# Optimization experiments

Measured on AMD Instinct MI355X. Metric: run time of the kernel, lower is better.

Reference implementation:

```python
import jax, jax.numpy as jnp
import numpy as np

C = 1536          # interim_dim
D2 = 2 * C        # 3072, fc_nlb dim
LN_EPS = 1e-5


def setup_inputs() -> dict:
    key = jax.random.key(0)
    ks = jax.random.split(key, 24)
    B, L = 32, 1024
    s = 0.02
    inp = {
        "x": jax.random.normal(ks[0], (B, C), dtype=jnp.float32),
        "lfb_feats": jax.random.normal(ks[1], (B, L, C), dtype=jnp.float32),
        # 1x1 Conv1d weights act as (C_out, C_in) matmuls
        "theta_w": jax.random.normal(ks[2], (C, C), dtype=jnp.float32) * s,
        "theta_b": jnp.zeros((C,), dtype=jnp.float32),
        "phi_w": jax.random.normal(ks[3], (C, C), dtype=jnp.float32) * s,
        "phi_b": jnp.zeros((C,), dtype=jnp.float32),
        "gi_w": jax.random.normal(ks[4], (C, C), dtype=jnp.float32) * s,
        "gi_b": jnp.zeros((C,), dtype=jnp.float32),
        "ln_g": jnp.ones((C,), dtype=jnp.float32),
        "ln_b": jnp.zeros((C,), dtype=jnp.float32),
        "fc_w": jax.random.normal(ks[5], (C, C), dtype=jnp.float32) * s,
        "fc_b": jnp.zeros((C,), dtype=jnp.float32),
        "fc_nlb_w": jax.random.normal(ks[6], (D2, D2), dtype=jnp.float32) * s,
        "fc_nlb_b": jnp.zeros((D2,), dtype=jnp.float32),
        "fc1_w": jax.random.normal(ks[7], (1, 1024), dtype=jnp.float32) * s,
        "fc1_b": jnp.zeros((1,), dtype=jnp.float32),
        "fc2_w": jax.random.normal(ks[8], (1, 1024), dtype=jnp.float32) * s,
        "fc2_b": jnp.zeros((1,), dtype=jnp.float32),
        "fc3_w": jax.random.normal(ks[9], (1, 1024), dtype=jnp.float32) * s,
        "fc3_b": jnp.zeros((1,), dtype=jnp.float32),
        "fct_w": jax.random.normal(ks[10], (1, D2), dtype=jnp.float32) * s,
        "fct_b": jnp.zeros((1,), dtype=jnp.float32),
    }
    return inp


def _layernorm(x, g, b):
    mu = jnp.mean(x, axis=-1, keepdims=True)
    var = jnp.mean(jnp.square(x - mu), axis=-1, keepdims=True)
    return (x - mu) * jax.lax.rsqrt(var + LN_EPS) * g + b


def reference(x, lfb_feats, theta_w, theta_b, phi_w, phi_b, gi_w, gi_b,
              ln_g, ln_b, fc_w, fc_b, fc_nlb_w, fc_nlb_b,
              fc1_w, fc1_b, fc2_w, fc2_b, fc3_w, fc3_b, fct_w, fct_b):
    # --- _NLBlock on feats = x.unsqueeze(1): query sequence length is 1 ---
    # note: scale = 1/sqrt(1/C) = sqrt(C) (as in the original code)
    scale = jnp.sqrt(jnp.asarray(C, dtype=x.dtype))
    theta = x @ theta_w.T + theta_b                       # (B, C)
    phi = lfb_feats @ phi_w.T + phi_b                     # (B, L, C)
    gi = lfb_feats @ gi_w.T + gi_b                        # (B, L, C)
    scores = jnp.einsum('bc,blc->bl', theta, phi) * scale  # (B, L)
    attn = jax.nn.softmax(scores, axis=-1)
    o = jnp.einsum('bl,blc->bc', attn, gi)                # (B, C)
    o = jax.nn.relu(_layernorm(o, ln_g, ln_b))
    o = o @ fc_w.T + fc_b                                 # dropout -> identity (eval)
    longterm = o + x                                      # residual, (B, C)

    # --- head ---
    feats = jnp.concatenate([x, longterm], axis=1)        # (B, 2C)
    feats = jax.nn.relu(feats @ fc_nlb_w.T + fc_nlb_b)    # dropout -> identity
    f1 = feats[:, :1024]
    f2 = feats[:, 1024:2048]
    f3 = feats[:, 2048:3072]
    p1 = f1 @ fc1_w.T + fc1_b
    p2 = f2 @ fc2_w.T + fc2_b
    p3 = f3 @ fc3_w.T + fc3_b
    pt = feats @ fct_w.T + fct_b
    return jnp.concatenate([p1, p2, p3, pt], axis=1)      # (B, 4)
```

## Files before the change

kernel.cpp:

```cpp
#include <hip/hip_runtime.h>
#include <math.h>

#define B 32
#define C 1536
#define D2 3072
#define L 1024
#define KC 64
#define CH 16
#define LPW 16

__device__ inline float dot4(float4 a, float4 b) {
    return a.x * b.x + a.y * b.y + a.z * b.z + a.w * b.w;
}
__device__ inline float4 ld4(const float* p) { return *(const float4*)p; }
__device__ inline void   st4(float* p, float4 v) { *(float4*)p = v; }

__device__ inline int sw(int row, int q) {
    return row * KC + ((q ^ ((row >> 2) & 7)) << 2);
}

__global__ __launch_bounds__(256) void init_k(float* __restrict__ theta, const float* __restrict__ tb,
                                              float* __restrict__ u,
                                              float* __restrict__ obuf, const float* __restrict__ gib,
                                              float* __restrict__ o2, const float* __restrict__ fcb,
                                              float* __restrict__ h, const float* __restrict__ fcnb) {
    int i = blockIdx.x * 256 + threadIdx.x;
    if (i < 32 * C) {
        int j = i % C;
        theta[i] = tb[j];
        u[i]     = 0.f;
        obuf[i]  = gib[j];
        o2[i]    = fcb[j];
    }
    if (i < 32 * D2) h[i] = fcnb[i % D2];
}

__global__ __launch_bounds__(256) void gemm32(const float* __restrict__ A,
                                              const float* __restrict__ W,
                                              float* __restrict__ out,
                                              int N, int K, int kchunks) {
    __shared__ float xs[32 * KC];
    __shared__ float wsm[64 * KC];
    int tid = threadIdx.x;
    int j0 = blockIdx.x * 64;
    int kb = blockIdx.y;
    int tb = tid & 15;
    int tj = tid >> 4;

    float4 acc0 = make_float4(0.f, 0.f, 0.f, 0.f);
    float4 acc1 = make_float4(0.f, 0.f, 0.f, 0.f);

    for (int c = 0; c < kchunks; ++c) {
        int k0 = (kb * kchunks + c) * KC;
        __syncthreads();
        #pragma unroll
        for (int p = 0; p < 2; ++p) {
            int f = tid + 256 * p;
            int row = f >> 4, q = f & 15;
            st4(xs + sw(row, q), ld4(A + (size_t)row * K + k0 + 4 * q));
        }
        #pragma unroll
        for (int p = 0; p < 4; ++p) {
            int f = tid + 256 * p;
            int row = f >> 4, q = f & 15;
            st4(wsm + sw(row, q), ld4(W + (size_t)(j0 + row) * K + k0 + 4 * q));
        }
        __syncthreads();
        #pragma unroll
        for (int kq = 0; kq < 16; ++kq) {
            float4 x0 = ld4(xs + sw(2 * tb, kq));
            float4 x1 = ld4(xs + sw(2 * tb + 1, kq));
            float4 w0 = ld4(wsm + sw(4 * tj + 0, kq));
            float4 w1 = ld4(wsm + sw(4 * tj + 1, kq));
            float4 w2 = ld4(wsm + sw(4 * tj + 2, kq));
            float4 w3 = ld4(wsm + sw(4 * tj + 3, kq));
            acc0.x += dot4(x0, w0); acc0.y += dot4(x0, w1);
            acc0.z += dot4(x0, w2); acc0.w += dot4(x0, w3);
            acc1.x += dot4(x1, w0); acc1.y += dot4(x1, w1);
            acc1.z += dot4(x1, w2); acc1.w += dot4(x1, w3);
        }
    }
    float* p0 = out + (size_t)(2 * tb + 0) * N + j0 + 4 * tj;
    float* p1 = out + (size_t)(2 * tb + 1) * N + j0 + 4 * tj;
    atomicAdd(p0 + 0, acc0.x); atomicAdd(p0 + 1, acc0.y);
    atomicAdd(p0 + 2, acc0.z); atomicAdd(p0 + 3, acc0.w);
    atomicAdd(p1 + 0, acc1.x); atomicAdd(p1 + 1, acc1.y);
    atomicAdd(p1 + 2, acc1.z); atomicAdd(p1 + 3, acc1.w);
}

__global__ __launch_bounds__(256) void gemm32_nt(const float* __restrict__ A,
                                                 const float* __restrict__ W,
                                                 float* __restrict__ out,
                                                 int N, int K, int kchunks) {
    __shared__ float xs[32 * KC];
    __shared__ float wsm[64 * KC];
    int tid = threadIdx.x;
    int j0 = blockIdx.x * 64;
    int kb = blockIdx.y;
    int tb = tid & 15;
    int tj = tid >> 4;

    float4 acc0 = make_float4(0.f, 0.f, 0.f, 0.f);
    float4 acc1 = make_float4(0.f, 0.f, 0.f, 0.f);

    for (int c = 0; c < kchunks; ++c) {
        int k0 = (kb * kchunks + c) * KC;
        __syncthreads();
        #pragma unroll
        for (int p = 0; p < 2; ++p) {
            int f = tid + 256 * p;
            int row = f >> 4, q = f & 15;
            st4(xs + sw(row, q), ld4(A + (size_t)row * K + k0 + 4 * q));
        }
        #pragma unroll
        for (int p = 0; p < 4; ++p) {
            int f = tid + 256 * p;
            int r = f >> 4;
            int cq = f & 15;
            float4 v = ld4(W + (size_t)(k0 + r) * N + j0 + 4 * cq);
            wsm[sw(4 * cq + 0, r >> 2) + (r & 3)] = v.x;
            wsm[sw(4 * cq + 1, r >> 2) + (r & 3)] = v.y;
            wsm[sw(4 * cq + 2, r >> 2) + (r & 3)] = v.z;
            wsm[sw(4 * cq + 3, r >> 2) + (r & 3)] = v.w;
        }
        __syncthreads();
        #pragma unroll
        for (int kq = 0; kq < 16; ++kq) {
            float4 x0 = ld4(xs + sw(2 * tb, kq));
            float4 x1 = ld4(xs + sw(2 * tb + 1, kq));
            float4 w0 = ld4(wsm + sw(4 * tj + 0, kq));
            float4 w1 = ld4(wsm + sw(4 * tj + 1, kq));
            float4 w2 = ld4(wsm + sw(4 * tj + 2, kq));
            float4 w3 = ld4(wsm + sw(4 * tj + 3, kq));
            acc0.x += dot4(x0, w0); acc0.y += dot4(x0, w1);
            acc0.z += dot4(x0, w2); acc0.w += dot4(x0, w3);
            acc1.x += dot4(x1, w0); acc1.y += dot4(x1, w1);
            acc1.z += dot4(x1, w2); acc1.w += dot4(x1, w3);
        }
    }
    float* p0 = out + (size_t)(2 * tb + 0) * N + j0 + 4 * tj;
    float* p1 = out + (size_t)(2 * tb + 1) * N + j0 + 4 * tj;
    atomicAdd(p0 + 0, acc0.x); atomicAdd(p0 + 1, acc0.y);
    atomicAdd(p0 + 2, acc0.z); atomicAdd(p0 + 3, acc0.w);
    atomicAdd(p1 + 0, acc1.x); atomicAdd(p1 + 1, acc1.y);
    atomicAdd(p1 + 2, acc1.z); atomicAdd(p1 + 3, acc1.w);
}

__global__ __launch_bounds__(256) void gemm32_h(const float* __restrict__ x,
                                                const float* __restrict__ o2,
                                                const float* __restrict__ W,
                                                float* __restrict__ out,
                                                int N, int K, int kchunks) {
    __shared__ float xs[32 * KC];
    __shared__ float wsm[64 * KC];
    int tid = threadIdx.x;
    int j0 = blockIdx.x * 64;
    int kb = blockIdx.y;
    int tb = tid & 15;
    int tj = tid >> 4;

    float4 acc0 = make_float4(0.f, 0.f, 0.f, 0.f);
    float4 acc1 = make_float4(0.f, 0.f, 0.f, 0.f);

    for (int c = 0; c < kchunks; ++c) {
        int k0 = (kb * kchunks + c) * KC;
        __syncthreads();
        #pragma unroll
        for (int p = 0; p < 2; ++p) {
            int f = tid + 256 * p;
            int row = f >> 4, q = f & 15;
            int kk = k0 + 4 * q;
            float4 v;
            if (kk < C) {
                v = ld4(x + (size_t)row * C + kk);
            } else {
                float4 a = ld4(x + (size_t)row * C + kk - C);
                float4 b = ld4(o2 + (size_t)row * C + kk - C);
                v = make_float4(a.x + b.x, a.y + b.y, a.z + b.z, a.w + b.w);
            }
            st4(xs + sw(row, q), v);
        }
        #pragma unroll
        for (int p = 0; p < 4; ++p) {
            int f = tid + 256 * p;
            int row = f >> 4, q = f & 15;
            st4(wsm + sw(row, q), ld4(W + (size_t)(j0 + row) * K + k0 + 4 * q));
        }
        __syncthreads();
        #pragma unroll
        for (int kq = 0; kq < 16; ++kq) {
            float4 x0 = ld4(xs + sw(2 * tb, kq));
            float4 x1 = ld4(xs + sw(2 * tb + 1, kq));
            float4 w0 = ld4(wsm + sw(4 * tj + 0, kq));
            float4 w1 = ld4(wsm + sw(4 * tj + 1, kq));
            float4 w2 = ld4(wsm + sw(4 * tj + 2, kq));
            float4 w3 = ld4(wsm + sw(4 * tj + 3, kq));
            acc0.x += dot4(x0, w0); acc0.y += dot4(x0, w1);
            acc0.z += dot4(x0, w2); acc0.w += dot4(x0, w3);
            acc1.x += dot4(x1, w0); acc1.y += dot4(x1, w1);
            acc1.z += dot4(x1, w2); acc1.w += dot4(x1, w3);
        }
    }
    float* p0 = out + (size_t)(2 * tb + 0) * N + j0 + 4 * tj;
    float* p1 = out + (size_t)(2 * tb + 1) * N + j0 + 4 * tj;
    atomicAdd(p0 + 0, acc0.x); atomicAdd(p0 + 1, acc0.y);
    atomicAdd(p0 + 2, acc0.z); atomicAdd(p0 + 3, acc0.w);
    atomicAdd(p1 + 0, acc1.x); atomicAdd(p1 + 1, acc1.y);
    atomicAdd(p1 + 2, acc1.z); atomicAdd(p1 + 3, acc1.w);
}

__global__ __launch_bounds__(256) void ln_relu(const float* __restrict__ obuf,
                                               const float* __restrict__ g,
                                               const float* __restrict__ bt,
                                               float* __restrict__ out) {
    int b = blockIdx.x, tid = threadIdx.x;
    __shared__ float r1[4], r2[4];
    float lv[6];
    float s1 = 0.f, s2 = 0.f;
    #pragma unroll
    for (int t = 0; t < 6; ++t) {
        int c = tid + 256 * t;
        float acc = obuf[(size_t)b * C + c];
        lv[t] = acc; s1 += acc; s2 += acc * acc;
    }
    #pragma unroll
    for (int off = 32; off > 0; off >>= 1) {
        s1 += __shfl_xor(s1, off, 64);
        s2 += __shfl_xor(s2, off, 64);
    }
    int wave = tid >> 6, lane = tid & 63;
    if (lane == 0) { r1[wave] = s1; r2[wave] = s2; }
    __syncthreads();
    s1 = r1[0] + r1[1] + r1[2] + r1[3];
    s2 = r2[0] + r2[1] + r2[2] + r2[3];
    float mu = s1 / (float)C;
    float var = s2 / (float)C - mu * mu;
    float rstd = 1.0f / sqrtf(var + 1e-5f);
    #pragma unroll
    for (int t = 0; t < 6; ++t) {
        int c = tid + 256 * t;
        float y = (lv[t] - mu) * rstd * g[c] + bt[c];
        out[(size_t)b * C + c] = fmaxf(y, 0.f);
    }
}

__global__ __launch_bounds__(256) void flash_k(const float* __restrict__ u,
                                               const float* __restrict__ lfb,
                                               float* __restrict__ pm,
                                               float* __restrict__ ps,
                                               float* __restrict__ pv) {
    int chunk = blockIdx.x;
    int b = blockIdx.y;
    int wave = threadIdx.x >> 6;
    int lane = threadIdx.x & 63;
    int widx = chunk * 4 + wave;

    const float scale = 39.19183588453085f;

    float uu[24];
    const float* ub = u + (size_t)b * C;
    #pragma unroll
    for (int t = 0; t < 6; ++t)
        *(float4*)(uu + 4 * t) = ld4(ub + 4 * lane + 256 * t);

    float m = -INFINITY, s = 0.f;
    float vv[24];
    #pragma unroll
    for (int t = 0; t < 24; ++t) vv[t] = 0.f;

    int l0 = chunk * (L / CH) + wave;
    for (int i = 0; i < LPW; ++i) {
        int l = l0 + i * 4;
        const float* row = lfb + ((size_t)b * L + l) * C;
        float xx[24];
        #pragma unroll
        for (int t = 0; t < 6; ++t)
            *(float4*)(xx + 4 * t) = ld4(row + 4 * lane + 256 * t);
        float d = 0.f;
        #pragma unroll
        for (int t = 0; t < 24; ++t) d += xx[t] * uu[t];
        #pragma unroll
        for (int off = 32; off > 0; off >>= 1) d += __shfl_xor(d, off, 64);
        float score = d * scale;
        float mn = fmaxf(m, score);
        float alpha = __expf(m - mn);
        float p = __expf(score - mn);
        s = s * alpha + p;
        #pragma unroll
        for (int t = 0; t < 24; ++t) vv[t] = vv[t] * alpha + p * xx[t];
        m = mn;
    }

    if (lane == 0) { pm[b * 64 + widx] = m; ps[b * 64 + widx] = s; }
    float* pvb = pv + ((size_t)b * 64 + widx) * C;
    #pragma unroll
    for (int t = 0; t < 6; ++t)
        st4(pvb + 4 * lane + 256 * t, *(float4*)(vv + 4 * t));
}

__global__ __launch_bounds__(256) void combine_k(const float* __restrict__ pm,
                                                 const float* __restrict__ ps,
                                                 const float* __restrict__ pv,
                                                 float* __restrict__ v) {
    int cc = blockIdx.x;
    int b = blockIdx.y;
    int tid = threadIdx.x;
    __shared__ float coef[64];
    if (tid < 64) {
        float mj = pm[b * 64 + tid];
        float M = mj;
        #pragma unroll
        for (int off = 32; off > 0; off >>= 1) M = fmaxf(M, __shfl_xor(M, off, 64));
        float ej = expf(mj - M);
        float S = ps[b * 64 + tid] * ej;
        #pragma unroll
        for (int off = 32; off > 0; off >>= 1) S += __shfl_xor(S, off, 64);
        coef[tid] = ej / S;
    }
    __syncthreads();
    int c = cc * 256 + tid;
    float acc = 0.f;
    #pragma unroll 8
    for (int j = 0; j < 64; ++j)
        acc += coef[j] * pv[((size_t)b * 64 + j) * C + c];
    v[(size_t)b * C + c] = acc;
}

__global__ __launch_bounds__(256) void final_k(const float* __restrict__ h,
                                               const float* __restrict__ w1, const float* __restrict__ b1,
                                               const float* __restrict__ w2, const float* __restrict__ b2,
                                               const float* __restrict__ w3, const float* __restrict__ b3,
                                               const float* __restrict__ wt, const float* __restrict__ bt,
                                               float* __restrict__ out) {
    int b = blockIdx.x;
    int tid = threadIdx.x;
    float ph0 = 0.f, ph1 = 0.f, ph2 = 0.f, ptv = 0.f;
    #pragma unroll
    for (int t = 0; t < 12; ++t) {
        int j = tid + 256 * t;
        float s = fmaxf(h[(size_t)b * D2 + j], 0.f);
        ptv += s * wt[j];
        int jj = tid + 256 * (t & 3);
        if (t < 4)       ph0 += s * w1[jj];
        else if (t < 8)  ph1 += s * w2[jj];
        else             ph2 += s * w3[jj];
    }
    #pragma unroll
    for (int off = 32; off > 0; off >>= 1) {
        ph0 += __shfl_xor(ph0, off, 64);
        ph1 += __shfl_xor(ph1, off, 64);
        ph2 += __shfl_xor(ph2, off, 64);
        ptv += __shfl_xor(ptv, off, 64);
    }
    __shared__ float red[4][4];
    int wave = tid >> 6, lane = tid & 63;
    if (lane == 0) {
        red[wave][0] = ph0; red[wave][1] = ph1; red[wave][2] = ph2; red[wave][3] = ptv;
    }
    __syncthreads();
    if (tid < 4) {
        float v = red[0][tid] + red[1][tid] + red[2][tid] + red[3][tid];
        float bias = (tid == 0) ? b1[0] : (tid == 1) ? b2[0] : (tid == 2) ? b3[0] : bt[0];
        out[b * 4 + tid] = v + bias;
    }
}

extern "C" void kernel_launch(void* const* d_in, const int* in_sizes, int n_in,
                              void* d_out, int out_size, void* d_ws, size_t ws_size,
                              hipStream_t stream) {
    (void)in_sizes; (void)n_in; (void)out_size; (void)ws_size;
    const float* x       = (const float*)d_in[0];
    const float* lfb     = (const float*)d_in[1];
    const float* theta_w = (const float*)d_in[2];
    const float* theta_b = (const float*)d_in[3];
    const float* phi_w   = (const float*)d_in[4];
    const float* gi_w    = (const float*)d_in[6];
    const float* gi_b    = (const float*)d_in[7];
    const float* ln_g    = (const float*)d_in[8];
    const float* ln_b    = (const float*)d_in[9];
    const float* fc_w    = (const float*)d_in[10];
    const float* fc_b    = (const float*)d_in[11];
    const float* fcn_w   = (const float*)d_in[12];
    const float* fcn_b   = (const float*)d_in[13];
    const float* w1 = (const float*)d_in[14]; const float* b1 = (const float*)d_in[15];
    const float* w2 = (const float*)d_in[16]; const float* b2 = (const float*)d_in[17];
    const float* w3 = (const float*)d_in[18]; const float* b3 = (const float*)d_in[19];
    const float* wt = (const float*)d_in[20]; const float* bt = (const float*)d_in[21];
    float* out = (float*)d_out;
    float* w = (float*)d_ws;

    float* pv    = w;
    float* pm    = w + 3145728;
    float* ps    = w + 3147776;
    float* theta = w + 3149824;
    float* u     = w + 3198976;
    float* vbuf  = w + 3248128;
    float* obuf  = w + 3297280;
    float* oln   = w + 3346432;
    float* o2    = w + 3395584;
    float* h     = w + 3444736;

    init_k<<<384, 256, 0, stream>>>(theta, theta_b, u, obuf, gi_b, o2, fc_b, h, fcn_b);

    gemm32<<<dim3(24, 12), 256, 0, stream>>>(x, theta_w, theta, C, C, 2);

    gemm32_nt<<<dim3(24, 12), 256, 0, stream>>>(theta, phi_w, u, C, C, 2);

    flash_k<<<dim3(CH, B), 256, 0, stream>>>(u, lfb, pm, ps, pv);
    combine_k<<<dim3(6, B), 256, 0, stream>>>(pm, ps, pv, vbuf);

    gemm32<<<dim3(24, 12), 256, 0, stream>>>(vbuf, gi_w, obuf, C, C, 2);
    ln_relu<<<B, 256, 0, stream>>>(obuf, ln_g, ln_b, oln);

    gemm32<<<dim3(24, 12), 256, 0, stream>>>(oln, fc_w, o2, C, C, 2);

    gemm32_h<<<dim3(48, 12), 256, 0, stream>>>(x, o2, fcn_w, h, D2, D2, 4);

    final_k<<<B, 256, 0, stream>>>(h, w1, b1, w2, b2, w3, b3, wt, bt, out);
}
```

Before: 477.7 us.

## Fuse all stages into one persistent megakernel with grid barriers

Replaces the sequence of separate kernel launches with a single persistent kernel of 512 blocks that runs every stage and separates them with atomic-counter grid barriers. Split-K GEMM results are no longer accumulated with global atomics into pre-initialised buffers. Each K-slice writes its own partial tile, and a reduction stage sums the slices and adds the bias, which also removes the init kernel. This is meant to cut launch and inter-kernel gaps and atomic traffic, at the cost of extra barrier stages, partial-buffer memory traffic, and reliance on all 512 blocks being co-resident (two per CU).

```diff
diff --git a/kernel.cpp b/kernel.cpp
--- a/kernel.cpp
+++ b/kernel.cpp
@@ -1,11 +1,12 @@
 #include <hip/hip_runtime.h>
 #include <math.h>
 
-#define B 32
 #define C 1536
 #define D2 3072
 #define L 1024
 #define KC 64
+#define NB 512
+#define NT 256
 #define CH 16
 #define LPW 16
 
@@ -19,50 +20,49 @@
     return row * KC + ((q ^ ((row >> 2) & 7)) << 2);
 }
 
-__global__ __launch_bounds__(256) void init_k(float* __restrict__ theta, const float* __restrict__ tb,
-                                              float* __restrict__ u,
-                                              float* __restrict__ obuf, const float* __restrict__ gib,
-                                              float* __restrict__ o2, const float* __restrict__ fcb,
-                                              float* __restrict__ h, const float* __restrict__ fcnb) {
-    int i = blockIdx.x * 256 + threadIdx.x;
-    if (i < 32 * C) {
-        int j = i % C;
-        theta[i] = tb[j];
-        u[i]     = 0.f;
-        obuf[i]  = gib[j];
-        o2[i]    = fcb[j];
-    }
-    if (i < 32 * D2) h[i] = fcnb[i % D2];
-}
-
-__global__ __launch_bounds__(256) void gemm32(const float* __restrict__ A,
-                                              const float* __restrict__ W,
-                                              float* __restrict__ out,
-                                              int N, int K, int kchunks) {
-    __shared__ float xs[32 * KC];
-    __shared__ float wsm[64 * KC];
+struct Params {
+    const float *x, *lfb, *theta_w, *theta_b, *phi_w, *gi_w, *gi_b;
+    const float *ln_g, *ln_b, *fc_w, *fc_b, *fcn_w, *fcn_b;
+    const float *w1, *b1, *w2, *b2, *w3, *b3, *wt, *bt;
+    float *out;
+    float *part, *partH, *pv, *pm, *ps, *theta, *u, *vbuf, *oln, *lt;
+    unsigned *bar;
+};
+
+__device__ inline void gridbar(unsigned* bar, int idx) {
+    __syncthreads();
+    if (threadIdx.x == 0) {
+        __threadfence();
+        __hip_atomic_fetch_add(&bar[idx], 1u, __ATOMIC_ACQ_REL, __HIP_MEMORY_SCOPE_AGENT);
+        int spins = 0;
+        while (__hip_atomic_load(&bar[idx], __ATOMIC_ACQUIRE, __HIP_MEMORY_SCOPE_AGENT) < NB) {
+            __builtin_amdgcn_s_sleep(4);
+            if (++spins > (1 << 20)) break;
+        }
+        __threadfence();
+    }
+    __syncthreads();
+}
+
+__device__ void gemm_nn(const float* __restrict__ A, const float* __restrict__ W,
+                        float* __restrict__ part, int N, int K, int kchunks,
+                        int jt, int kb, float* xs, float* wsm) {
     int tid = threadIdx.x;
-    int j0 = blockIdx.x * 64;
-    int kb = blockIdx.y;
-    int tb = tid & 15;
-    int tj = tid >> 4;
-
+    int j0 = jt * 64;
+    int tb = tid & 15, tj = tid >> 4;
     float4 acc0 = make_float4(0.f, 0.f, 0.f, 0.f);
     float4 acc1 = make_float4(0.f, 0.f, 0.f, 0.f);
-
     for (int c = 0; c < kchunks; ++c) {
         int k0 = (kb * kchunks + c) * KC;
         __syncthreads();
         #pragma unroll
         for (int p = 0; p < 2; ++p) {
-            int f = tid + 256 * p;
-            int row = f >> 4, q = f & 15;
+            int f = tid + 256 * p, row = f >> 4, q = f & 15;
             st4(xs + sw(row, q), ld4(A + (size_t)row * K + k0 + 4 * q));
         }
         #pragma unroll
         for (int p = 0; p < 4; ++p) {
-            int f = tid + 256 * p;
-            int row = f >> 4, q = f & 15;
+            int f = tid + 256 * p, row = f >> 4, q = f & 15;
             st4(wsm + sw(row, q), ld4(W + (size_t)(j0 + row) * K + k0 + 4 * q));
         }
         __syncthreads();
@@ -80,36 +80,24 @@
             acc1.z += dot4(x1, w2); acc1.w += dot4(x1, w3);
         }
     }
-    float* p0 = out + (size_t)(2 * tb + 0) * N + j0 + 4 * tj;
-    float* p1 = out + (size_t)(2 * tb + 1) * N + j0 + 4 * tj;
-    atomicAdd(p0 + 0, acc0.x); atomicAdd(p0 + 1, acc0.y);
-    atomicAdd(p0 + 2, acc0.z); atomicAdd(p0 + 3, acc0.w);
-    atomicAdd(p1 + 0, acc1.x); atomicAdd(p1 + 1, acc1.y);
-    atomicAdd(p1 + 2, acc1.z); atomicAdd(p1 + 3, acc1.w);
-}
-
-__global__ __launch_bounds__(256) void gemm32_nt(const float* __restrict__ A,
-                                                 const float* __restrict__ W,
-                                                 float* __restrict__ out,
-                                                 int N, int K, int kchunks) {
-    __shared__ float xs[32 * KC];
-    __shared__ float wsm[64 * KC];
+    st4(part + ((size_t)kb * 32 + 2 * tb + 0) * N + j0 + 4 * tj, acc0);
+    st4(part + ((size_t)kb * 32 + 2 * tb + 1) * N + j0 + 4 * tj, acc1);
+}
+
+__device__ void gemm_nt(const float* __restrict__ A, const float* __restrict__ W,
+                        float* __restrict__ part, int N, int K, int kchunks,
+                        int jt, int kb, float* xs, float* wsm) {
     int tid = threadIdx.x;
-    int j0 = blockIdx.x * 64;
-    int kb = blockIdx.y;
-    int tb = tid & 15;
-    int tj = tid >> 4;
-
+    int j0 = jt * 64;
+    int tb = tid & 15, tj = tid >> 4;
     float4 acc0 = make_float4(0.f, 0.f, 0.f, 0.f);
     float4 acc1 = make_float4(0.f, 0.f, 0.f, 0.f);
-
     for (int c = 0; c < kchunks; ++c) {
         int k0 = (kb * kchunks + c) * KC;
         __syncthreads();
         #pragma unroll
         for (int p = 0; p < 2; ++p) {
-            int f = tid + 256 * p;
-            int row = f >> 4, q = f & 15;
+            int f = tid + 256 * p, row = f >> 4, q = f & 15;
             st4(xs + sw(row, q), ld4(A + (size_t)row * K + k0 + 4 * q));
         }
         #pragma unroll
@@ -138,53 +126,33 @@
             acc1.z += dot4(x1, w2); acc1.w += dot4(x1, w3);
         }
     }
-    float* p0 = out + (size_t)(2 * tb + 0) * N + j0 + 4 * tj;
-    float* p1 = out + (size_t)(2 * tb + 1) * N + j0 + 4 * tj;
-    atomicAdd(p0 + 0, acc0.x); atomicAdd(p0 + 1, acc0.y);
-    atomicAdd(p0 + 2, acc0.z); atomicAdd(p0 + 3, acc0.w);
-    atomicAdd(p1 + 0, acc1.x); atomicAdd(p1 + 1, acc1.y);
-    atomicAdd(p1 + 2, acc1.z); atomicAdd(p1 + 3, acc1.w);
-}
-
-__global__ __launch_bounds__(256) void gemm32_h(const float* __restrict__ x,
-                                                const float* __restrict__ o2,
-                                                const float* __restrict__ W,
-                                                float* __restrict__ out,
-                                                int N, int K, int kchunks) {
-    __shared__ float xs[32 * KC];
-    __shared__ float wsm[64 * KC];
+    st4(part + ((size_t)kb * 32 + 2 * tb + 0) * N + j0 + 4 * tj, acc0);
+    st4(part + ((size_t)kb * 32 + 2 * tb + 1) * N + j0 + 4 * tj, acc1);
+}
+
+__device__ void gemm_feats(const float* __restrict__ x, const float* __restrict__ lt,
+                           const float* __restrict__ W, float* __restrict__ part,
+                           int jt, int kb, float* xs, float* wsm) {
     int tid = threadIdx.x;
-    int j0 = blockIdx.x * 64;
-    int kb = blockIdx.y;
-    int tb = tid & 15;
-    int tj = tid >> 4;
-
+    int j0 = jt * 64;
+    int tb = tid & 15, tj = tid >> 4;
     float4 acc0 = make_float4(0.f, 0.f, 0.f, 0.f);
     float4 acc1 = make_float4(0.f, 0.f, 0.f, 0.f);
-
-    for (int c = 0; c < kchunks; ++c) {
-        int k0 = (kb * kchunks + c) * KC;
+    for (int c = 0; c < 4; ++c) {
+        int k0 = (kb * 4 + c) * KC;
         __syncthreads();
         #pragma unroll
         for (int p = 0; p < 2; ++p) {
-            int f = tid + 256 * p;
-            int row = f >> 4, q = f & 15;
+            int f = tid + 256 * p, row = f >> 4, q = f & 15;
             int kk = k0 + 4 * q;
-            float4 v;
-            if (kk < C) {
-                v = ld4(x + (size_t)row * C + kk);
-            } else {
-                float4 a = ld4(x + (size_t)row * C + kk - C);
-                float4 b = ld4(o2 + (size_t)row * C + kk - C);
-                v = make_float4(a.x + b.x, a.y + b.y, a.z + b.z, a.w + b.w);
-            }
+            float4 v = (kk < C) ? ld4(x + (size_t)row * C + kk)
+                                : ld4(lt + (size_t)row * C + kk - C);
             st4(xs + sw(row, q), v);
         }
         #pragma unroll
         for (int p = 0; p < 4; ++p) {
-            int f = tid + 256 * p;
-            int row = f >> 4, q = f & 15;
-            st4(wsm + sw(row, q), ld4(W + (size_t)(j0 + row) * K + k0 + 4 * q));
+            int f = tid + 256 * p, row = f >> 4, q = f & 15;
+            st4(wsm + sw(row, q), ld4(W + (size_t)(j0 + row) * D2 + k0 + 4 * q));
         }
         __syncthreads();
         #pragma unroll
@@ -201,26 +169,108 @@
             acc1.z += dot4(x1, w2); acc1.w += dot4(x1, w3);
         }
     }
-    float* p0 = out + (size_t)(2 * tb + 0) * N + j0 + 4 * tj;
-    float* p1 = out + (size_t)(2 * tb + 1) * N + j0 + 4 * tj;
-    atomicAdd(p0 + 0, acc0.x); atomicAdd(p0 + 1, acc0.y);
-    atomicAdd(p0 + 2, acc0.z); atomicAdd(p0 + 3, acc0.w);
-    atomicAdd(p1 + 0, acc1.x); atomicAdd(p1 + 1, acc1.y);
-    atomicAdd(p1 + 2, acc1.z); atomicAdd(p1 + 3, acc1.w);
-}
-
-__global__ __launch_bounds__(256) void ln_relu(const float* __restrict__ obuf,
-                                               const float* __restrict__ g,
-                                               const float* __restrict__ bt,
-                                               float* __restrict__ out) {
+    st4(part + ((size_t)kb * 32 + 2 * tb + 0) * D2 + j0 + 4 * tj, acc0);
+    st4(part + ((size_t)kb * 32 + 2 * tb + 1) * D2 + j0 + 4 * tj, acc1);
+}
+
+__device__ inline void reduce12(const float* __restrict__ part, const float* __restrict__ bias,
+                                const float* __restrict__ addx, float* __restrict__ outp) {
+    int i = blockIdx.x * NT + threadIdx.x;
+    if (i < 32 * C) {
+        int b = i / C, j = i - b * C;
+        float s = 0.f;
+        #pragma unroll
+        for (int kk = 0; kk < 12; ++kk) s += part[((size_t)kk * 32 + b) * C + j];
+        if (bias) s += bias[j];
+        if (addx) s += addx[i];
+        outp[i] = s;
+    }
+}
+
+__device__ void flash_stage(const Params& p) {
+    int gid = blockIdx.x;
+    int b = gid & 31, chunk = gid >> 5;
+    int wave = threadIdx.x >> 6, lane = threadIdx.x & 63;
+    int widx = chunk * 4 + wave;
+
+    const float scale = 39.19183588453085f;
+
+    float uu[24];
+    const float* ub = p.u + (size_t)b * C;
+    #pragma unroll
+    for (int t = 0; t < 6; ++t)
+        *(float4*)(uu + 4 * t) = ld4(ub + 4 * lane + 256 * t);
+
+    float m = -INFINITY, s = 0.f;
+    float vv[24];
+    #pragma unroll
+    for (int t = 0; t < 24; ++t) vv[t] = 0.f;
+
+    int l0 = chunk * (L / CH) + wave;
+    for (int i = 0; i < LPW; ++i) {
+        int l = l0 + i * 4;
+        const float* row = p.lfb + ((size_t)b * L + l) * C;
+        float xx[24];
+        #pragma unroll
+        for (int t = 0; t < 6; ++t)
+            *(float4*)(xx + 4 * t) = ld4(row + 4 * lane + 256 * t);
+        float d = 0.f;
+        #pragma unroll
+        for (int t = 0; t < 24; ++t) d += xx[t] * uu[t];
+        #pragma unroll
+        for (int off = 32; off > 0; off >>= 1) d += __shfl_xor(d, off, 64);
+        float score = d * scale;
+        float mn = fmaxf(m, score);
+        float alpha = __expf(m - mn);
+        float pr = __expf(score - mn);
+        s = s * alpha + pr;
+        #pragma unroll
+        for (int t = 0; t < 24; ++t) vv[t] = vv[t] * alpha + pr * xx[t];
+        m = mn;
+    }
+
+    if (lane == 0) { p.pm[b * 64 + widx] = m; p.ps[b * 64 + widx] = s; }
+    float* pvb = p.pv + ((size_t)b * 64 + widx) * C;
+    #pragma unroll
+    for (int t = 0; t < 6; ++t)
+        st4(pvb + 4 * lane + 256 * t, *(float4*)(vv + 4 * t));
+}
+
+__device__ void combine_stage(const Params& p, float* coef) {
+    int gid = blockIdx.x;
+    int b = gid & 31, cc = gid >> 5;
+    int tid = threadIdx.x;
+    if (tid < 64) {
+        float mj = p.pm[b * 64 + tid];
+        float M = mj;
+        #pragma unroll
+        for (int off = 32; off > 0; off >>= 1) M = fmaxf(M, __shfl_xor(M, off, 64));
+        float ej = expf(mj - M);
+        float S = p.ps[b * 64 + tid] * ej;
+        #pragma unroll
+        for (int off = 32; off > 0; off >>= 1) S += __shfl_xor(S, off, 64);
+        coef[tid] = ej / S;
+    }
+    __syncthreads();
+    int c = cc * 256 + tid;
+    float acc = 0.f;
+    #pragma unroll 8
+    for (int j = 0; j < 64; ++j)
+        acc += coef[j] * p.pv[((size_t)b * 64 + j) * C + c];
+    p.vbuf[(size_t)b * C + c] = acc;
+}
+
+__device__ void ln_stage(const Params& p, float* r1, float* r2) {
     int b = blockIdx.x, tid = threadIdx.x;
-    __shared__ float r1[4], r2[4];
     float lv[6];
     float s1 = 0.f, s2 = 0.f;
     #pragma unroll
     for (int t = 0; t < 6; ++t) {
         int c = tid + 256 * t;
-        float acc = obuf[(size_t)b * C + c];
+        float acc = 0.f;
+        #pragma unroll
+        for (int kk = 0; kk < 12; ++kk) acc += p.part[((size_t)kk * 32 + b) * C + c];
+        acc += p.gi_b[c];
         lv[t] = acc; s1 += acc; s2 += acc * acc;
     }
     #pragma unroll
@@ -239,111 +289,28 @@
     #pragma unroll
     for (int t = 0; t < 6; ++t) {
         int c = tid + 256 * t;
-        float y = (lv[t] - mu) * rstd * g[c] + bt[c];
-        out[(size_t)b * C + c] = fmaxf(y, 0.f);
-    }
-}
-
-__global__ __launch_bounds__(256) void flash_k(const float* __restrict__ u,
-                                               const float* __restrict__ lfb,
-                                               float* __restrict__ pm,
-                                               float* __restrict__ ps,
-                                               float* __restrict__ pv) {
-    int chunk = blockIdx.x;
-    int b = blockIdx.y;
-    int wave = threadIdx.x >> 6;
-    int lane = threadIdx.x & 63;
-    int widx = chunk * 4 + wave;
-
-    const float scale = 39.19183588453085f;
-
-    float uu[24];
-    const float* ub = u + (size_t)b * C;
-    #pragma unroll
-    for (int t = 0; t < 6; ++t)
-        *(float4*)(uu + 4 * t) = ld4(ub + 4 * lane + 256 * t);
-
-    float m = -INFINITY, s = 0.f;
-    float vv[24];
-    #pragma unroll
-    for (int t = 0; t < 24; ++t) vv[t] = 0.f;
-
-    int l0 = chunk * (L / CH) + wave;
-    for (int i = 0; i < LPW; ++i) {
-        int l = l0 + i * 4;
-        const float* row = lfb + ((size_t)b * L + l) * C;
-        float xx[24];
-        #pragma unroll
-        for (int t = 0; t < 6; ++t)
-            *(float4*)(xx + 4 * t) = ld4(row + 4 * lane + 256 * t);
-        float d = 0.f;
-        #pragma unroll
-        for (int t = 0; t < 24; ++t) d += xx[t] * uu[t];
-        #pragma unroll
-        for (int off = 32; off > 0; off >>= 1) d += __shfl_xor(d, off, 64);
-        float score = d * scale;
-        float mn = fmaxf(m, score);
-        float alpha = __expf(m - mn);
-        float p = __expf(score - mn);
-        s = s * alpha + p;
-        #pragma unroll
-        for (int t = 0; t < 24; ++t) vv[t] = vv[t] * alpha + p * xx[t];
-        m = mn;
-    }
-
-    if (lane == 0) { pm[b * 64 + widx] = m; ps[b * 64 + widx] = s; }
-    float* pvb = pv + ((size_t)b * 64 + widx) * C;
-    #pragma unroll
-    for (int t = 0; t < 6; ++t)
-        st4(pvb + 4 * lane + 256 * t, *(float4*)(vv + 4 * t));
-}
-
-__global__ __launch_bounds__(256) void combine_k(const float* __restrict__ pm,
-                                                 const float* __restrict__ ps,
-                                                 const float* __restrict__ pv,
-                                                 float* __restrict__ v) {
-    int cc = blockIdx.x;
-    int b = blockIdx.y;
-    int tid = threadIdx.x;
-    __shared__ float coef[64];
-    if (tid < 64) {
-        float mj = pm[b * 64 + tid];
-        float M = mj;
-        #pragma unroll
-        for (int off = 32; off > 0; off >>= 1) M = fmaxf(M, __shfl_xor(M, off, 64));
-        float ej = expf(mj - M);
-        float S = ps[b * 64 + tid] * ej;
-        #pragma unroll
-        for (int off = 32; off > 0; off >>= 1) S += __shfl_xor(S, off, 64);
-        coef[tid] = ej / S;
-    }
-    __syncthreads();
-    int c = cc * 256 + tid;
-    float acc = 0.f;
-    #pragma unroll 8
-    for (int j = 0; j < 64; ++j)
-        acc += coef[j] * pv[((size_t)b * 64 + j) * C + c];
-    v[(size_t)b * C + c] = acc;
-}
-
-__global__ __launch_bounds__(256) void final_k(const float* __restrict__ h,
-                                               const float* __restrict__ w1, const float* __restrict__ b1,
-                                               const float* __restrict__ w2, const float* __restrict__ b2,
-                                               const float* __restrict__ w3, const float* __restrict__ b3,
-                                               const float* __restrict__ wt, const float* __restrict__ bt,
-                                               float* __restrict__ out) {
-    int b = blockIdx.x;
-    int tid = threadIdx.x;
+        float y = (lv[t] - mu) * rstd * p.ln_g[c] + p.ln_b[c];
+        p.oln[(size_t)b * C + c] = fmaxf(y, 0.f);
+    }
+}
+
+__device__ void final_stage(const Params& p, float* red) {
+    int b = blockIdx.x, tid = threadIdx.x;
     float ph0 = 0.f, ph1 = 0.f, ph2 = 0.f, ptv = 0.f;
     #pragma unroll
     for (int t = 0; t < 12; ++t) {
         int j = tid + 256 * t;
-        float s = fmaxf(h[(size_t)b * D2 + j], 0.f);
-        ptv += s * wt[j];
+        float s = 0.f;
+        #pragma unroll
+        for (int ss = 0; ss < 12; ++ss)
+            s += p.partH[((size_t)ss * 32 + b) * D2 + j];
+        s += p.fcn_b[j];
+        s = fmaxf(s, 0.f);
+        ptv += s * p.wt[j];
         int jj = tid + 256 * (t & 3);
-        if (t < 4)       ph0 += s * w1[jj];
-        else if (t < 8)  ph1 += s * w2[jj];
-        else             ph2 += s * w3[jj];
+        if (t < 4)       ph0 += s * p.w1[jj];
+        else if (t < 8)  ph1 += s * p.w2[jj];
+        else             ph2 += s * p.w3[jj];
     }
     #pragma unroll
     for (int off = 32; off > 0; off >>= 1) {
@@ -352,69 +319,90 @@
         ph2 += __shfl_xor(ph2, off, 64);
         ptv += __shfl_xor(ptv, off, 64);
     }
-    __shared__ float red[4][4];
     int wave = tid >> 6, lane = tid & 63;
     if (lane == 0) {
-        red[wave][0] = ph0; red[wave][1] = ph1; red[wave][2] = ph2; red[wave][3] = ptv;
+        red[wave * 4 + 0] = ph0; red[wave * 4 + 1] = ph1;
+        red[wave * 4 + 2] = ph2; red[wave * 4 + 3] = ptv;
     }
     __syncthreads();
     if (tid < 4) {
-        float v = red[0][tid] + red[1][tid] + red[2][tid] + red[3][tid];
-        float bias = (tid == 0) ? b1[0] : (tid == 1) ? b2[0] : (tid == 2) ? b3[0] : bt[0];
-        out[b * 4 + tid] = v + bias;
-    }
+        float v = red[0 * 4 + tid] + red[1 * 4 + tid] + red[2 * 4 + tid] + red[3 * 4 + tid];
+        float bias = (tid == 0) ? p.b1[0] : (tid == 1) ? p.b2[0] : (tid == 2) ? p.b3[0] : p.bt[0];
+        p.out[b * 4 + tid] = v + bias;
+    }
+}
+
+__global__ __launch_bounds__(NT, 2) void mega(Params p) {
+    __shared__ float smem[6144];
+    float* xs = smem;
+    float* wsm = smem + 2048;
+    int gid = blockIdx.x;
+
+    if (gid < 288) gemm_nn(p.x, p.theta_w, p.part, C, C, 2, gid / 12, gid % 12, xs, wsm);
+    gridbar(p.bar, 0);
+    reduce12(p.part, p.theta_b, nullptr, p.theta);
+    gridbar(p.bar, 1);
+    if (gid < 288) gemm_nt(p.theta, p.phi_w, p.part, C, C, 2, gid / 12, gid % 12, xs, wsm);
+    gridbar(p.bar, 2);
+    reduce12(p.part, nullptr, nullptr, p.u);
+    gridbar(p.bar, 3);
+    flash_stage(p);
+    gridbar(p.bar, 4);
+    if (gid < 192) combine_stage(p, smem);
+    gridbar(p.bar, 5);
+    if (gid < 288) gemm_nn(p.vbuf, p.gi_w, p.part, C, C, 2, gid / 12, gid % 12, xs, wsm);
+    gridbar(p.bar, 6);
+    if (gid < 32) ln_stage(p, smem, smem + 8);
+    gridbar(p.bar, 7);
+    if (gid < 288) gemm_nn(p.oln, p.fc_w, p.part, C, C, 2, gid / 12, gid % 12, xs, wsm);
+    gridbar(p.bar, 8);
+    reduce12(p.part, p.fc_b, p.x, p.lt);
+    gridbar(p.bar, 9);
+    for (int t = gid; t < 576; t += NB)
+        gemm_feats(p.x, p.lt, p.fcn_w, p.partH, t / 12, t % 12, xs, wsm);
+    gridbar(p.bar, 10);
+    if (gid < 32) final_stage(p, smem);
 }
 
 extern "C" void kernel_launch(void* const* d_in, const int* in_sizes, int n_in,
                               void* d_out, int out_size, void* d_ws, size_t ws_size,
                               hipStream_t stream) {
     (void)in_sizes; (void)n_in; (void)out_size; (void)ws_size;
-    const float* x       = (const float*)d_in[0];
-    const float* lfb     = (const float*)d_in[1];
-    const float* theta_w = (const float*)d_in[2];
-    const float* theta_b = (const float*)d_in[3];
-    const float* phi_w   = (const float*)d_in[4];
-    const float* gi_w    = (const float*)d_in[6];
-    const float* gi_b    = (const float*)d_in[7];
-    const float* ln_g    = (const float*)d_in[8];
-    const float* ln_b    = (const float*)d_in[9];
-    const float* fc_w    = (const float*)d_in[10];
-    const float* fc_b    = (const float*)d_in[11];
-    const float* fcn_w   = (const float*)d_in[12];
-    const float* fcn_b   = (const float*)d_in[13];
-    const float* w1 = (const float*)d_in[14]; const float* b1 = (const float*)d_in[15];
-    const float* w2 = (const float*)d_in[16]; const float* b2 = (const float*)d_in[17];
-    const float* w3 = (const float*)d_in[18]; const float* b3 = (const float*)d_in[19];
-    const float* wt = (const float*)d_in[20]; const float* bt = (const float*)d_in[21];
-    float* out = (float*)d_out;
     float* w = (float*)d_ws;
 
-    float* pv    = w;
-    float* pm    = w + 3145728;
-    float* ps    = w + 3147776;
-    float* theta = w + 3149824;
-    float* u     = w + 3198976;
-    float* vbuf  = w + 3248128;
-    float* obuf  = w + 3297280;
-    float* oln   = w + 3346432;
-    float* o2    = w + 3395584;
-    float* h     = w + 3444736;
-
-    init_k<<<384, 256, 0, stream>>>(theta, theta_b, u, obuf, gi_b, o2, fc_b, h, fcn_b);
-
-    gemm32<<<dim3(24, 12), 256, 0, stream>>>(x, theta_w, theta, C, C, 2);
-
-    gemm32_nt<<<dim3(24, 12), 256, 0, stream>>>(theta, phi_w, u, C, C, 2);
-
-    flash_k<<<dim3(CH, B), 256, 0, stream>>>(u, lfb, pm, ps, pv);
-    combine_k<<<dim3(6, B), 256, 0, stream>>>(pm, ps, pv, vbuf);
-
-    gemm32<<<dim3(24, 12), 256, 0, stream>>>(vbuf, gi_w, obuf, C, C, 2);
-    ln_relu<<<B, 256, 0, stream>>>(obuf, ln_g, ln_b, oln);
-
-    gemm32<<<dim3(24, 12), 256, 0, stream>>>(oln, fc_w, o2, C, C, 2);
-
-    gemm32_h<<<dim3(48, 12), 256, 0, stream>>>(x, o2, fcn_w, h, D2, D2, 4);
-
-    final_k<<<B, 256, 0, stream>>>(h, w1, b1, w2, b2, w3, b3, wt, bt, out);
-}
+    Params p;
+    p.x       = (const float*)d_in[0];
+    p.lfb     = (const float*)d_in[1];
+    p.theta_w = (const float*)d_in[2];
+    p.theta_b = (const float*)d_in[3];
+    p.phi_w   = (const float*)d_in[4];
+    p.gi_w    = (const float*)d_in[6];
+    p.gi_b    = (const float*)d_in[7];
+    p.ln_g    = (const float*)d_in[8];
+    p.ln_b    = (const float*)d_in[9];
+    p.fc_w    = (const float*)d_in[10];
+    p.fc_b    = (const float*)d_in[11];
+    p.fcn_w   = (const float*)d_in[12];
+    p.fcn_b   = (const float*)d_in[13];
+    p.w1 = (const float*)d_in[14]; p.b1 = (const float*)d_in[15];
+    p.w2 = (const float*)d_in[16]; p.b2 = (const float*)d_in[17];
+    p.w3 = (const float*)d_in[18]; p.b3 = (const float*)d_in[19];
+    p.wt = (const float*)d_in[20]; p.bt = (const float*)d_in[21];
+    p.out = (float*)d_out;
+
+    p.part  = w;
+    p.partH = w + 589824;
+    p.pv    = w + 1769472;
+    p.pm    = w + 4915200;
+    p.ps    = w + 4917248;
+    p.theta = w + 4919296;
+    p.u     = w + 4968448;
+    p.vbuf  = w + 5017600;
+    p.oln   = w + 5066752;
+    p.lt    = w + 5115904;
+    p.bar   = (unsigned*)(w + 5165056);
+
+    hipMemsetAsync((void*)p.bar, 0, 64, stream);
+
+    mega<<<dim3(NB), dim3(NT), 0, stream>>>(p);
+}
```

After: 1.458 ms. +205.2%, slower.

## Replace atomic split-K accumulation with partial buffers reduced in consumer kernels

Applied to the files above, without the earlier changes.

Each split-K GEMM now writes its per-slice partial sums to a dedicated buffer instead of atomically adding into a pre-initialized output. The 12-way reduction plus bias is folded into the loading stage of the next kernel (gemm_u, flash_k, reduce_ln_relu, gemm_h, final_k), and the init kernel is removed. This removes atomic traffic and one launch. In exchange, every consumer re-reads 12 partials, several times over across blocks, which adds memory traffic.

```diff
diff --git a/kernel.cpp b/kernel.cpp
--- a/kernel.cpp
+++ b/kernel.cpp
@@ -19,25 +19,19 @@
     return row * KC + ((q ^ ((row >> 2) & 7)) << 2);
 }
 
-__global__ __launch_bounds__(256) void init_k(float* __restrict__ theta, const float* __restrict__ tb,
-                                              float* __restrict__ u,
-                                              float* __restrict__ obuf, const float* __restrict__ gib,
-                                              float* __restrict__ o2, const float* __restrict__ fcb,
-                                              float* __restrict__ h, const float* __restrict__ fcnb) {
-    int i = blockIdx.x * 256 + threadIdx.x;
-    if (i < 32 * C) {
-        int j = i % C;
-        theta[i] = tb[j];
-        u[i]     = 0.f;
-        obuf[i]  = gib[j];
-        o2[i]    = fcb[j];
-    }
-    if (i < 32 * D2) h[i] = fcnb[i % D2];
+__device__ inline float4 sum12(const float* __restrict__ part, int row, int col, int N) {
+    float4 s = ld4(part + (size_t)row * N + col);
+    #pragma unroll
+    for (int kk = 1; kk < 12; ++kk) {
+        float4 t = ld4(part + ((size_t)kk * 32 + row) * N + col);
+        s.x += t.x; s.y += t.y; s.z += t.z; s.w += t.w;
+    }
+    return s;
 }
 
 __global__ __launch_bounds__(256) void gemm32(const float* __restrict__ A,
                                               const float* __restrict__ W,
-                                              float* __restrict__ out,
+                                              float* __restrict__ part,
                                               int N, int K, int kchunks) {
     __shared__ float xs[32 * KC];
     __shared__ float wsm[64 * KC];
@@ -80,44 +74,43 @@
             acc1.z += dot4(x1, w2); acc1.w += dot4(x1, w3);
         }
     }
-    float* p0 = out + (size_t)(2 * tb + 0) * N + j0 + 4 * tj;
-    float* p1 = out + (size_t)(2 * tb + 1) * N + j0 + 4 * tj;
-    atomicAdd(p0 + 0, acc0.x); atomicAdd(p0 + 1, acc0.y);
-    atomicAdd(p0 + 2, acc0.z); atomicAdd(p0 + 3, acc0.w);
-    atomicAdd(p1 + 0, acc1.x); atomicAdd(p1 + 1, acc1.y);
-    atomicAdd(p1 + 2, acc1.z); atomicAdd(p1 + 3, acc1.w);
-}
-
-__global__ __launch_bounds__(256) void gemm32_nt(const float* __restrict__ A,
-                                                 const float* __restrict__ W,
-                                                 float* __restrict__ out,
-                                                 int N, int K, int kchunks) {
+    st4(part + ((size_t)kb * 32 + 2 * tb + 0) * N + j0 + 4 * tj, acc0);
+    st4(part + ((size_t)kb * 32 + 2 * tb + 1) * N + j0 + 4 * tj, acc1);
+}
+
+__global__ __launch_bounds__(256) void gemm_u(const float* __restrict__ pT,
+                                              const float* __restrict__ tb_,
+                                              const float* __restrict__ W,
+                                              float* __restrict__ part) {
     __shared__ float xs[32 * KC];
     __shared__ float wsm[64 * KC];
     int tid = threadIdx.x;
     int j0 = blockIdx.x * 64;
     int kb = blockIdx.y;
-    int tb = tid & 15;
-    int tj = tid >> 4;
+    int tb = tid & 15, tj = tid >> 4;
 
     float4 acc0 = make_float4(0.f, 0.f, 0.f, 0.f);
     float4 acc1 = make_float4(0.f, 0.f, 0.f, 0.f);
 
-    for (int c = 0; c < kchunks; ++c) {
-        int k0 = (kb * kchunks + c) * KC;
+    for (int c = 0; c < 2; ++c) {
+        int k0 = (kb * 2 + c) * KC;
         __syncthreads();
         #pragma unroll
         for (int p = 0; p < 2; ++p) {
             int f = tid + 256 * p;
             int row = f >> 4, q = f & 15;
-            st4(xs + sw(row, q), ld4(A + (size_t)row * K + k0 + 4 * q));
+            int col = k0 + 4 * q;
+            float4 v = sum12(pT, row, col, C);
+            float4 b4 = ld4(tb_ + col);
+            v.x += b4.x; v.y += b4.y; v.z += b4.z; v.w += b4.w;
+            st4(xs + sw(row, q), v);
         }
         #pragma unroll
         for (int p = 0; p < 4; ++p) {
             int f = tid + 256 * p;
             int r = f >> 4;
             int cq = f & 15;
-            float4 v = ld4(W + (size_t)(k0 + r) * N + j0 + 4 * cq);
+            float4 v = ld4(W + (size_t)(k0 + r) * C + j0 + 4 * cq);
             wsm[sw(4 * cq + 0, r >> 2) + (r & 3)] = v.x;
             wsm[sw(4 * cq + 1, r >> 2) + (r & 3)] = v.y;
             wsm[sw(4 * cq + 2, r >> 2) + (r & 3)] = v.z;
@@ -138,32 +131,27 @@
             acc1.z += dot4(x1, w2); acc1.w += dot4(x1, w3);
         }
     }
-    float* p0 = out + (size_t)(2 * tb + 0) * N + j0 + 4 * tj;
-    float* p1 = out + (size_t)(2 * tb + 1) * N + j0 + 4 * tj;
-    atomicAdd(p0 + 0, acc0.x); atomicAdd(p0 + 1, acc0.y);
-    atomicAdd(p0 + 2, acc0.z); atomicAdd(p0 + 3, acc0.w);
-    atomicAdd(p1 + 0, acc1.x); atomicAdd(p1 + 1, acc1.y);
-    atomicAdd(p1 + 2, acc1.z); atomicAdd(p1 + 3, acc1.w);
-}
-
-__global__ __launch_bounds__(256) void gemm32_h(const float* __restrict__ x,
-                                                const float* __restrict__ o2,
-                                                const float* __restrict__ W,
-                                                float* __restrict__ out,
-                                                int N, int K, int kchunks) {
+    st4(part + ((size_t)kb * 32 + 2 * tb + 0) * C + j0 + 4 * tj, acc0);
+    st4(part + ((size_t)kb * 32 + 2 * tb + 1) * C + j0 + 4 * tj, acc1);
+}
+
+__global__ __launch_bounds__(256) void gemm_h(const float* __restrict__ x,
+                                              const float* __restrict__ pF,
+                                              const float* __restrict__ fcb,
+                                              const float* __restrict__ W,
+                                              float* __restrict__ part) {
     __shared__ float xs[32 * KC];
     __shared__ float wsm[64 * KC];
     int tid = threadIdx.x;
     int j0 = blockIdx.x * 64;
     int kb = blockIdx.y;
-    int tb = tid & 15;
-    int tj = tid >> 4;
+    int tb = tid & 15, tj = tid >> 4;
 
     float4 acc0 = make_float4(0.f, 0.f, 0.f, 0.f);
     float4 acc1 = make_float4(0.f, 0.f, 0.f, 0.f);
 
-    for (int c = 0; c < kchunks; ++c) {
-        int k0 = (kb * kchunks + c) * KC;
+    for (int c = 0; c < 4; ++c) {
+        int k0 = (kb * 4 + c) * KC;
         __syncthreads();
         #pragma unroll
         for (int p = 0; p < 2; ++p) {
@@ -174,9 +162,14 @@
             if (kk < C) {
                 v = ld4(x + (size_t)row * C + kk);
             } else {
-                float4 a = ld4(x + (size_t)row * C + kk - C);
-                float4 b = ld4(o2 + (size_t)row * C + kk - C);
-                v = make_float4(a.x + b.x, a.y + b.y, a.z + b.z, a.w + b.w);
+                int col = kk - C;
+                float4 s = sum12(pF, row, col, C);
+                float4 b4 = ld4(fcb + col);
+                float4 xa = ld4(x + (size_t)row * C + col);
+                v.x = (s.x + b4.x) + xa.x;
+                v.y = (s.y + b4.y) + xa.y;
+                v.z = (s.z + b4.z) + xa.z;
+                v.w = (s.w + b4.w) + xa.w;
             }
             st4(xs + sw(row, q), v);
         }
@@ -184,7 +177,7 @@
         for (int p = 0; p < 4; ++p) {
             int f = tid + 256 * p;
             int row = f >> 4, q = f & 15;
-            st4(wsm + sw(row, q), ld4(W + (size_t)(j0 + row) * K + k0 + 4 * q));
+            st4(wsm + sw(row, q), ld4(W + (size_t)(j0 + row) * D2 + k0 + 4 * q));
         }
         __syncthreads();
         #pragma unroll
@@ -201,18 +194,15 @@
             acc1.z += dot4(x1, w2); acc1.w += dot4(x1, w3);
         }
     }
-    float* p0 = out + (size_t)(2 * tb + 0) * N + j0 + 4 * tj;
-    float* p1 = out + (size_t)(2 * tb + 1) * N + j0 + 4 * tj;
-    atomicAdd(p0 + 0, acc0.x); atomicAdd(p0 + 1, acc0.y);
-    atomicAdd(p0 + 2, acc0.z); atomicAdd(p0 + 3, acc0.w);
-    atomicAdd(p1 + 0, acc1.x); atomicAdd(p1 + 1, acc1.y);
-    atomicAdd(p1 + 2, acc1.z); atomicAdd(p1 + 3, acc1.w);
-}
-
-__global__ __launch_bounds__(256) void ln_relu(const float* __restrict__ obuf,
-                                               const float* __restrict__ g,
-                                               const float* __restrict__ bt,
-                                               float* __restrict__ out) {
+    st4(part + ((size_t)kb * 32 + 2 * tb + 0) * D2 + j0 + 4 * tj, acc0);
+    st4(part + ((size_t)kb * 32 + 2 * tb + 1) * D2 + j0 + 4 * tj, acc1);
+}
+
+__global__ __launch_bounds__(256) void reduce_ln_relu(const float* __restrict__ part,
+                                                      const float* __restrict__ bias,
+                                                      const float* __restrict__ g,
+                                                      const float* __restrict__ bt,
+                                                      float* __restrict__ out) {
     int b = blockIdx.x, tid = threadIdx.x;
     __shared__ float r1[4], r2[4];
     float lv[6];
@@ -220,7 +210,10 @@
     #pragma unroll
     for (int t = 0; t < 6; ++t) {
         int c = tid + 256 * t;
-        float acc = obuf[(size_t)b * C + c];
+        float acc = 0.f;
+        #pragma unroll
+        for (int kk = 0; kk < 12; ++kk) acc += part[((size_t)kk * 32 + b) * C + c];
+        acc += bias[c];
         lv[t] = acc; s1 += acc; s2 += acc * acc;
     }
     #pragma unroll
@@ -244,24 +237,35 @@
     }
 }
 
-__global__ __launch_bounds__(256) void flash_k(const float* __restrict__ u,
+__global__ __launch_bounds__(256) void flash_k(const float* __restrict__ pU,
                                                const float* __restrict__ lfb,
                                                float* __restrict__ pm,
                                                float* __restrict__ ps,
                                                float* __restrict__ pv) {
+    __shared__ float u_lds[C];
     int chunk = blockIdx.x;
     int b = blockIdx.y;
-    int wave = threadIdx.x >> 6;
-    int lane = threadIdx.x & 63;
+    int tid = threadIdx.x;
+    int wave = tid >> 6;
+    int lane = tid & 63;
     int widx = chunk * 4 + wave;
 
     const float scale = 39.19183588453085f;
 
+    #pragma unroll
+    for (int t = 0; t < 6; ++t) {
+        int cc = tid + 256 * t;
+        float s = 0.f;
+        #pragma unroll
+        for (int kk = 0; kk < 12; ++kk) s += pU[((size_t)kk * 32 + b) * C + cc];
+        u_lds[cc] = s;
+    }
+    __syncthreads();
+
     float uu[24];
-    const float* ub = u + (size_t)b * C;
     #pragma unroll
     for (int t = 0; t < 6; ++t)
-        *(float4*)(uu + 4 * t) = ld4(ub + 4 * lane + 256 * t);
+        *(float4*)(uu + 4 * t) = ld4(u_lds + 4 * lane + 256 * t);
 
     float m = -INFINITY, s = 0.f;
     float vv[24];
@@ -326,7 +330,8 @@
     v[(size_t)b * C + c] = acc;
 }
 
-__global__ __launch_bounds__(256) void final_k(const float* __restrict__ h,
+__global__ __launch_bounds__(256) void final_k(const float* __restrict__ partH,
+                                               const float* __restrict__ fcn_b,
                                                const float* __restrict__ w1, const float* __restrict__ b1,
                                                const float* __restrict__ w2, const float* __restrict__ b2,
                                                const float* __restrict__ w3, const float* __restrict__ b3,
@@ -338,7 +343,12 @@
     #pragma unroll
     for (int t = 0; t < 12; ++t) {
         int j = tid + 256 * t;
-        float s = fmaxf(h[(size_t)b * D2 + j], 0.f);
+        float s = 0.f;
+        #pragma unroll
+        for (int ss = 0; ss < 12; ++ss)
+            s += partH[((size_t)ss * 32 + b) * D2 + j];
+        s += fcn_b[j];
+        s = fmaxf(s, 0.f);
         ptv += s * wt[j];
         int jj = tid + 256 * (t & 3);
         if (t < 4)       ph0 += s * w1[jj];
@@ -389,32 +399,32 @@
     float* out = (float*)d_out;
     float* w = (float*)d_ws;
 
-    float* pv    = w;
-    float* pm    = w + 3145728;
-    float* ps    = w + 3147776;
-    float* theta = w + 3149824;
-    float* u     = w + 3198976;
-    float* vbuf  = w + 3248128;
-    float* obuf  = w + 3297280;
-    float* oln   = w + 3346432;
-    float* o2    = w + 3395584;
-    float* h     = w + 3444736;
-
-    init_k<<<384, 256, 0, stream>>>(theta, theta_b, u, obuf, gi_b, o2, fc_b, h, fcn_b);
-
-    gemm32<<<dim3(24, 12), 256, 0, stream>>>(x, theta_w, theta, C, C, 2);
-
-    gemm32_nt<<<dim3(24, 12), 256, 0, stream>>>(theta, phi_w, u, C, C, 2);
-
-    flash_k<<<dim3(CH, B), 256, 0, stream>>>(u, lfb, pm, ps, pv);
+    float* partT = w;
+    float* partU = w + 589824;
+    float* partG = w + 1179648;
+    float* partF = w + 1769472;
+    float* partH = w + 2359296;
+    float* pv    = w + 3538944;
+    float* pm    = w + 6684672;
+    float* ps    = w + 6686720;
+    float* vbuf  = w + 6688768;
+    float* oln   = w + 6737920;
+
+    gemm32<<<dim3(24, 12), 256, 0, stream>>>(x, theta_w, partT, C, C, 2);
+
+    gemm_u<<<dim3(24, 12), 256, 0, stream>>>(partT, theta_b, phi_w, partU);
+
+    flash_k<<<dim3(CH, B), 256, 0, stream>>>(partU, lfb, pm, ps, pv);
+
     combine_k<<<dim3(6, B), 256, 0, stream>>>(pm, ps, pv, vbuf);
 
-    gemm32<<<dim3(24, 12), 256, 0, stream>>>(vbuf, gi_w, obuf, C, C, 2);
-    ln_relu<<<B, 256, 0, stream>>>(obuf, ln_g, ln_b, oln);
-
-    gemm32<<<dim3(24, 12), 256, 0, stream>>>(oln, fc_w, o2, C, C, 2);
-
-    gemm32_h<<<dim3(48, 12), 256, 0, stream>>>(x, o2, fcn_w, h, D2, D2, 4);
-
-    final_k<<<B, 256, 0, stream>>>(h, w1, b1, w2, b2, w3, b3, wt, bt, out);
-}
+    gemm32<<<dim3(24, 12), 256, 0, stream>>>(vbuf, gi_w, partG, C, C, 2);
+
+    reduce_ln_relu<<<B, 256, 0, stream>>>(partG, gi_b, ln_g, ln_b, oln);
+
+    gemm32<<<dim3(24, 12), 256, 0, stream>>>(oln, fc_w, partF, C, C, 2);
+
+    gemm_h<<<dim3(48, 12), 256, 0, stream>>>(x, partF, fc_b, fcn_w, partH);
+
+    final_k<<<B, 256, 0, stream>>>(partH, fcn_b, w1, b1, w2, b2, w3, b3, wt, bt, out);
+}
```

Result: slower. 488.7 us (+2.3%).
